# Kernel optimization log

Hardware: AMD Instinct MI355X
Metric: run time of the kernel (lower is better)

## Reference

```python
import jax, jax.numpy as jnp
import numpy as np

EMBED_DIM = 4
SEQ_LEN = 14 * 14


def setup_inputs() -> dict:
    key = jax.random.key(0)
    ks = jax.random.split(key, 7)
    B = 32768
    x = jax.random.normal(ks[0], (B, 1, 28, 28), dtype=jnp.float32)
    conv_w = jax.random.normal(ks[1], (4, 1, 2, 2), dtype=jnp.float32) * 0.5
    conv_b = jax.random.normal(ks[2], (4,), dtype=jnp.float32) * 0.1
    rotation_params = jax.random.uniform(ks[3], (16,), dtype=jnp.float32)
    entangle_params = jax.random.uniform(ks[4], (16,), dtype=jnp.float32)
    lin_w = jax.random.normal(ks[5], (10, 784), dtype=jnp.float32) * 0.05
    lin_b = jax.random.normal(ks[6], (10,), dtype=jnp.float32) * 0.05
    return {"x": x, "conv_w": conv_w, "conv_b": conv_b,
            "rotation_params": rotation_params, "entangle_params": entangle_params,
            "lin_w": lin_w, "lin_b": lin_b}


def reference(x, conv_w, conv_b, rotation_params, entangle_params, lin_w, lin_b):
    B = x.shape[0]
    # Quanvolution filter: Conv2d(1,4,k=2,s=2) -> [B,4,14,14]
    feat = jax.lax.conv_general_dilated(
        x, conv_w, window_strides=(2, 2), padding='VALID',
        dimension_numbers=('NCHW', 'OIHW', 'NCHW'))
    feat = feat + conv_b[None, :, None, None]
    # flatten (channel-major like torch .view) then reshape to [B, 196, 4]
    feat = feat.reshape(B, -1).reshape(B, SEQ_LEN, EMBED_DIM)
    # mean embedding per sample: [B, 4]
    mean_embeds = feat.mean(axis=1)
    # classical self-attention on a length-1 sequence per sample
    R = rotation_params.reshape(EMBED_DIM, EMBED_DIM)
    E = entangle_params.reshape(EMBED_DIM, EMBED_DIM)
    q = mean_embeds @ R                               # [B, 4]
    k = mean_embeds @ E                               # [B, 4]
    scores = jnp.einsum('bd,bd->b', q, k) / jnp.sqrt(jnp.float32(EMBED_DIM))
    # softmax over a single-element axis (seq_len == 1) -> all ones, kept for fidelity
    scores = jax.nn.softmax(scores[:, None], axis=-1)  # [B, 1]
    attn_weights = scores * mean_embeds                # [B, 4] (== mean_embeds)
    # broadcast-scale features and classify
    feat = (feat * attn_weights[:, None, :]).reshape(B, -1)  # [B, 784]
    logits = feat @ lin_w.T + lin_b
    return jax.nn.log_softmax(logits, axis=-1)
```

## Files before the change

### kernel.cpp

```cpp
#include <hip/hip_runtime.h>


typedef __attribute__((ext_vector_type(8))) short bf16x8;
typedef __attribute__((ext_vector_type(4))) float f32x4;
typedef __attribute__((ext_vector_type(4))) unsigned int uint4v;

union BU { uint4v u; bf16x8 b; };
union AB { unsigned int u[4]; bf16x8 b; };

__device__ __forceinline__ unsigned rne16(float f) {
  const unsigned u = __float_as_uint(f);
  return (u + 0x7FFFu + ((u >> 16) & 1u)) >> 16;
}

#define CST_F 19200
#define A_F   19240

__global__ void qsac_prep(const float* __restrict__ cw, const float* __restrict__ cb,
                          const float* __restrict__ lw, float* __restrict__ wsf) {
  unsigned short* gt = (unsigned short*)wsf;
  const int i = blockIdx.x * 256 + threadIdx.x;
  const int e = i & 7, ln = (i >> 3) & 63, c = i >> 9;
  const int t = c / 3, nt = c - t * 3;
  const int col = nt * 16 + (ln & 15);
  const int k = t * 32 + (ln >> 4) * 8 + e;
  float val = 0.f;
  if (k < 784) {
    const int r = k / 28, cc = k - r * 28;
    const int kh = r & 1, kw = cc & 1;
    const int p = (r >> 1) * 14 + (cc >> 1);
    const int dpix = (2 * ((r >> 1) & 1) + (cc >> 1)) & 3;
    const int cd = col / 12, cj = col - cd * 12;
    if (cd == dpix) {
      const float w0 = cw[(kh << 1) + kw],     w1 = cw[4 + (kh << 1) + kw],
                  w2 = cw[8 + (kh << 1) + kw], w3 = cw[12 + (kh << 1) + kw];
      if (cj < 10)
        val = w0 * lw[cj * 784 + p]       + w1 * lw[cj * 784 + 196 + p] +
              w2 * lw[cj * 784 + 392 + p] + w3 * lw[cj * 784 + 588 + p];
      else if (cj == 10)
        val = (w0 + w1 + w2 + w3) * (1.0f / 196.0f);
    }
  }
  gt[c * 512 + ln * 8 + e] = (unsigned short)rne16(val);

  if (blockIdx.x == 0) {
    const int u = threadIdx.x;
    if (u < 40) {
      const int d = u / 10, j = u - (u / 10) * 10;
      const float b0 = cb[0], b1 = cb[1], b2 = cb[2], b3 = cb[3];
      float s = 0.f;
#pragma unroll 7
      for (int q = d; q < 196; q += 4)
        s += b0 * lw[j * 784 + q]       + b1 * lw[j * 784 + 196 + q] +
             b2 * lw[j * 784 + 392 + q] + b3 * lw[j * 784 + 588 + q];
      wsf[CST_F + u] = s;
    } else if (u == 40) {
      wsf[A_F] = (cb[0] + cb[1] + cb[2] + cb[3]) * 0.25f;
    }
  }
}

__global__ __launch_bounds__(512)
__attribute__((amdgpu_waves_per_eu(4, 4))) void qsac_main(
    const float* __restrict__ x, const float* __restrict__ wsf,
    const float* __restrict__ lin_b, float* __restrict__ out) {
  __shared__ unsigned int smemu[19200];

  const int tid = threadIdx.x;
  const int lane = tid & 63;
  const int wid = __builtin_amdgcn_readfirstlane(tid >> 6);
  const int strip = wid & 3;
  const int khalf = wid >> 2;
  const int nn = lane & 15, kb = lane >> 4;
  const int sbase = blockIdx.x * 64 + strip * 16;
  const float* xrow = x + (size_t)(sbase + nn) * 784;

  {
    const char* wsb = (const char*)wsf;
#pragma unroll
    for (int i = 0; i < 10; ++i) {
      const int c = i * 8 + wid;
      if (c < 75) {
        __builtin_amdgcn_global_load_lds(
            (const __attribute__((address_space(1))) unsigned int*)
                (wsb + (size_t)(c * 64 + lane) * 16),
            (__attribute__((address_space(3))) unsigned int*)&smemu[c * 256],
            16, 0, 0);
      }
    }
  }
  __syncthreads();

  f32x4 acc[3];
#pragma unroll
  for (int nt = 0; nt < 3; ++nt) acc[nt] = (f32x4){0.f, 0.f, 0.f, 0.f};

  auto tile = [&](const float4& a, const float4& b2, int t) {
    BU bh[3];
    const unsigned int* bb = smemu + t * 768 + lane * 4;
#pragma unroll
    for (int nt = 0; nt < 3; ++nt) bh[nt].u = *(const uint4v*)(bb + nt * 256);
    AB Ah;
    Ah.u[0] = rne16(a.x)  | (rne16(a.y)  << 16);
    Ah.u[1] = rne16(a.z)  | (rne16(a.w)  << 16);
    Ah.u[2] = rne16(b2.x) | (rne16(b2.y) << 16);
    Ah.u[3] = rne16(b2.z) | (rne16(b2.w) << 16);
#pragma unroll
    for (int nt = 0; nt < 3; ++nt)
      acc[nt] = __builtin_amdgcn_mfma_f32_16x16x32_bf16(Ah.b, bh[nt].b, acc[nt], 0, 0, 0);
  };

  auto ldA = [&](int t, float4& a, float4& b2) {
    const int ka = t * 32 + kb * 8;
    const int kc = (ka < 784) ? ka : 0;
    a = *(const float4*)(xrow + kc);
    b2 = *(const float4*)(xrow + kc + 4);
  };

  const int t0 = khalf ? 12 : 0;
  const int t1 = khalf ? 25 : 12;
  float4 xa, xb, na, nb;
  ldA(t0, xa, xb);
#pragma unroll 1
  for (int t = t0; t < t1 - 1; ++t) {
    ldA(t + 1, na, nb);
    tile(xa, xb, t);
    xa = na; xb = nb;
  }
  tile(xa, xb, t1 - 1);

  __syncthreads();
  float* red = (float*)smemu;
  if (khalf == 1) {
#pragma unroll
    for (int nt = 0; nt < 3; ++nt)
#pragma unroll
      for (int rg = 0; rg < 4; ++rg)
        red[(strip * 64 + lane) * 12 + nt * 4 + rg] = acc[nt][rg];
  }
  __syncthreads();
  if (khalf == 0) {
#pragma unroll
    for (int nt = 0; nt < 3; ++nt)
#pragma unroll
      for (int rg = 0; rg < 4; ++rg)
        acc[nt][rg] += red[(strip * 64 + lane) * 12 + nt * 4 + rg];

    float* cx = (float*)smemu + 3072 + strip * (16 * 52);
#pragma unroll
    for (int nt = 0; nt < 3; ++nt)
#pragma unroll
      for (int rg = 0; rg < 4; ++rg)
        cx[(kb * 4 + rg) * 52 + nt * 16 + nn] = acc[nt][rg];
    __builtin_amdgcn_wave_barrier();

    if (lane < 16) {
      float Y[48];
#pragma unroll
      for (int q = 0; q < 12; ++q) {
        const float4 t4 = *(const float4*)&cx[lane * 52 + q * 4];
        Y[q * 4 + 0] = t4.x; Y[q * 4 + 1] = t4.y;
        Y[q * 4 + 2] = t4.z; Y[q * 4 + 3] = t4.w;
      }
      const float a = wsf[A_F];
      float M[4];
#pragma unroll
      for (int d = 0; d < 4; ++d) M[d] = a + Y[d * 12 + 10];
      float logits[10];
#pragma unroll
      for (int j = 0; j < 10; ++j) {
        float vv = lin_b[j];
#pragma unroll
        for (int d = 0; d < 4; ++d)
          vv += M[d] * (wsf[CST_F + d * 10 + j] + Y[d * 12 + j]);
        logits[j] = vv;
      }
      float mx = logits[0];
#pragma unroll
      for (int j = 1; j < 10; ++j) mx = fmaxf(mx, logits[j]);
      float se = 0.f;
#pragma unroll
      for (int j = 0; j < 10; ++j) se += __expf(logits[j] - mx);
      const float lse = mx + __logf(se);
      float* op = out + (size_t)(sbase + lane) * 10;
#pragma unroll
      for (int j = 0; j < 10; ++j) op[j] = logits[j] - lse;
    }
  }
}

extern "C" void kernel_launch(void* const* d_in, const int* in_sizes, int n_in,
                              void* d_out, int out_size, void* d_ws, size_t ws_size,
                              hipStream_t stream) {
  (void)n_in; (void)ws_size; (void)out_size;
  const float* x = (const float*)d_in[0];
  const float* conv_w = (const float*)d_in[1];
  const float* conv_b = (const float*)d_in[2];
  const float* lin_w = (const float*)d_in[5];
  const float* lin_b = (const float*)d_in[6];
  float* out = (float*)d_out;
  float* wsf = (float*)d_ws;

  hipLaunchKernelGGL(qsac_prep, dim3(150), dim3(256), 0, stream,
                     conv_w, conv_b, lin_w, wsf);

  const int B = in_sizes[0] / 784;
  const int nblk = B / 64;
  hipLaunchKernelGGL(qsac_main, dim3(nblk), dim3(512), 0, stream,
                     x, wsf, lin_b, out);
}
```

Before: 29.46 us.

## Switch to 32x32x16 MFMA with 128-sample blocks and 4-way K split

Replaces the 16x16x32 bf16 MFMA tiles with 32x32x16 MFMAs. Each block now handles 128 samples with 1024 threads: 4 strips of 32 rows and 4 K-quarters reduced through LDS. The prep kernel re-lays out the folded weight matrix into 64-column, 16-K slabs, dropping the padded-N third tile in favour of two 32-wide tiles. The aim is fewer MFMA issues and better reuse per B fragment. In exchange it adds a larger LDS footprint, a bigger cross-wave reduction with an extra barrier, and higher per-thread accumulator register pressure.

Result: slower. 32.70 us (+11.0%).

```diff
diff --git a/kernel.cpp b/kernel.cpp
--- a/kernel.cpp
+++ b/kernel.cpp
@@ -2,7 +2,7 @@
 
 
 typedef __attribute__((ext_vector_type(8))) short bf16x8;
-typedef __attribute__((ext_vector_type(4))) float f32x4;
+typedef __attribute__((ext_vector_type(16))) float f32x16;
 typedef __attribute__((ext_vector_type(4))) unsigned int uint4v;
 
 union BU { uint4v u; bf16x8 b; };
@@ -13,19 +13,19 @@
   return (u + 0x7FFFu + ((u >> 16) & 1u)) >> 16;
 }
 
-#define CST_F 19200
-#define A_F   19240
+#define CST_F 25088
+#define A_F   25128
 
 __global__ void qsac_prep(const float* __restrict__ cw, const float* __restrict__ cb,
                           const float* __restrict__ lw, float* __restrict__ wsf) {
   unsigned short* gt = (unsigned short*)wsf;
   const int i = blockIdx.x * 256 + threadIdx.x;
   const int e = i & 7, ln = (i >> 3) & 63, c = i >> 9;
-  const int t = c / 3, nt = c - t * 3;
-  const int col = nt * 16 + (ln & 15);
-  const int k = t * 32 + (ln >> 4) * 8 + e;
+  const int s = c >> 1, nt = c & 1;
+  const int col = nt * 32 + (ln & 31);
+  const int k = s * 16 + (ln >> 5) * 8 + e;
   float val = 0.f;
-  if (k < 784) {
+  if (col < 48) {
     const int r = k / 28, cc = k - r * 28;
     const int kh = r & 1, kw = cc & 1;
     const int p = (r >> 1) * 14 + (cc >> 1);
@@ -48,39 +48,40 @@
     if (u < 40) {
       const int d = u / 10, j = u - (u / 10) * 10;
       const float b0 = cb[0], b1 = cb[1], b2 = cb[2], b3 = cb[3];
-      float s = 0.f;
+      float s2 = 0.f;
 #pragma unroll 7
       for (int q = d; q < 196; q += 4)
-        s += b0 * lw[j * 784 + q]       + b1 * lw[j * 784 + 196 + q] +
-             b2 * lw[j * 784 + 392 + q] + b3 * lw[j * 784 + 588 + q];
-      wsf[CST_F + u] = s;
+        s2 += b0 * lw[j * 784 + q]       + b1 * lw[j * 784 + 196 + q] +
+              b2 * lw[j * 784 + 392 + q] + b3 * lw[j * 784 + 588 + q];
+      wsf[CST_F + u] = s2;
     } else if (u == 40) {
       wsf[A_F] = (cb[0] + cb[1] + cb[2] + cb[3]) * 0.25f;
     }
   }
 }
 
-__global__ __launch_bounds__(512)
+__global__ __launch_bounds__(1024)
 __attribute__((amdgpu_waves_per_eu(4, 4))) void qsac_main(
     const float* __restrict__ x, const float* __restrict__ wsf,
     const float* __restrict__ lin_b, float* __restrict__ out) {
-  __shared__ unsigned int smemu[19200];
+  __shared__ unsigned int smemu[25088];
 
   const int tid = threadIdx.x;
   const int lane = tid & 63;
   const int wid = __builtin_amdgcn_readfirstlane(tid >> 6);
   const int strip = wid & 3;
-  const int khalf = wid >> 2;
-  const int nn = lane & 15, kb = lane >> 4;
-  const int sbase = blockIdx.x * 64 + strip * 16;
+  const int kq = wid >> 2;
+  const int nn = lane & 31;
+  const int g = lane >> 5;
+  const int sbase = blockIdx.x * 128 + strip * 32;
   const float* xrow = x + (size_t)(sbase + nn) * 784;
 
   {
     const char* wsb = (const char*)wsf;
 #pragma unroll
-    for (int i = 0; i < 10; ++i) {
-      const int c = i * 8 + wid;
-      if (c < 75) {
+    for (int i = 0; i < 7; ++i) {
+      const int c = i * 16 + wid;
+      if (c < 98) {
         __builtin_amdgcn_global_load_lds(
             (const __attribute__((address_space(1))) unsigned int*)
                 (wsb + (size_t)(c * 64 + lane) * 16),
@@ -91,74 +92,75 @@
   }
   __syncthreads();
 
-  f32x4 acc[3];
-#pragma unroll
-  for (int nt = 0; nt < 3; ++nt) acc[nt] = (f32x4){0.f, 0.f, 0.f, 0.f};
-
-  auto tile = [&](const float4& a, const float4& b2, int t) {
-    BU bh[3];
-    const unsigned int* bb = smemu + t * 768 + lane * 4;
-#pragma unroll
-    for (int nt = 0; nt < 3; ++nt) bh[nt].u = *(const uint4v*)(bb + nt * 256);
+  f32x16 acc0, acc1;
+#pragma unroll
+  for (int r = 0; r < 16; ++r) { acc0[r] = 0.f; acc1[r] = 0.f; }
+
+  auto tile = [&](const float4& a, const float4& b2, int s) {
+    BU bh0, bh1;
+    const unsigned int* bb = smemu + s * 512 + lane * 4;
+    bh0.u = *(const uint4v*)bb;
+    bh1.u = *(const uint4v*)(bb + 256);
     AB Ah;
     Ah.u[0] = rne16(a.x)  | (rne16(a.y)  << 16);
     Ah.u[1] = rne16(a.z)  | (rne16(a.w)  << 16);
     Ah.u[2] = rne16(b2.x) | (rne16(b2.y) << 16);
     Ah.u[3] = rne16(b2.z) | (rne16(b2.w) << 16);
-#pragma unroll
-    for (int nt = 0; nt < 3; ++nt)
-      acc[nt] = __builtin_amdgcn_mfma_f32_16x16x32_bf16(Ah.b, bh[nt].b, acc[nt], 0, 0, 0);
+    acc0 = __builtin_amdgcn_mfma_f32_32x32x16_bf16(Ah.b, bh0.b, acc0, 0, 0, 0);
+    acc1 = __builtin_amdgcn_mfma_f32_32x32x16_bf16(Ah.b, bh1.b, acc1, 0, 0, 0);
   };
 
-  auto ldA = [&](int t, float4& a, float4& b2) {
-    const int ka = t * 32 + kb * 8;
-    const int kc = (ka < 784) ? ka : 0;
-    a = *(const float4*)(xrow + kc);
-    b2 = *(const float4*)(xrow + kc + 4);
+  auto ldA = [&](int s, float4& a, float4& b2) {
+    const float* p = xrow + s * 16 + g * 8;
+    a = *(const float4*)p;
+    b2 = *(const float4*)(p + 4);
   };
 
-  const int t0 = khalf ? 12 : 0;
-  const int t1 = khalf ? 25 : 12;
+  const int s0 = (kq == 0) ? 0 : 13 + (kq - 1) * 12;
+  const int s1 = s0 + ((kq == 0) ? 13 : 12);
   float4 xa, xb, na, nb;
-  ldA(t0, xa, xb);
+  ldA(s0, xa, xb);
 #pragma unroll 1
-  for (int t = t0; t < t1 - 1; ++t) {
-    ldA(t + 1, na, nb);
-    tile(xa, xb, t);
+  for (int s = s0; s < s1 - 1; ++s) {
+    ldA(s + 1, na, nb);
+    tile(xa, xb, s);
     xa = na; xb = nb;
   }
-  tile(xa, xb, t1 - 1);
+  tile(xa, xb, s1 - 1);
 
   __syncthreads();
   float* red = (float*)smemu;
-  if (khalf == 1) {
-#pragma unroll
-    for (int nt = 0; nt < 3; ++nt)
-#pragma unroll
-      for (int rg = 0; rg < 4; ++rg)
-        red[(strip * 64 + lane) * 12 + nt * 4 + rg] = acc[nt][rg];
-  }
-  __syncthreads();
-  if (khalf == 0) {
-#pragma unroll
-    for (int nt = 0; nt < 3; ++nt)
-#pragma unroll
-      for (int rg = 0; rg < 4; ++rg)
-        acc[nt][rg] += red[(strip * 64 + lane) * 12 + nt * 4 + rg];
-
-    float* cx = (float*)smemu + 3072 + strip * (16 * 52);
-#pragma unroll
-    for (int nt = 0; nt < 3; ++nt)
-#pragma unroll
-      for (int rg = 0; rg < 4; ++rg)
-        cx[(kb * 4 + rg) * 52 + nt * 16 + nn] = acc[nt][rg];
+  if (kq > 0) {
+    float* rp = red + ((strip * 3 + (kq - 1)) * 64 + lane) * 32;
+#pragma unroll
+    for (int r = 0; r < 16; ++r) { rp[r] = acc0[r]; rp[16 + r] = acc1[r]; }
+  }
+  __syncthreads();
+  if (kq == 0) {
+#pragma unroll
+    for (int q = 0; q < 3; ++q) {
+      const float* rp = red + ((strip * 3 + q) * 64 + lane) * 32;
+#pragma unroll
+      for (int r = 0; r < 16; ++r) { acc0[r] += rp[r]; acc1[r] += rp[16 + r]; }
+    }
+  }
+  __syncthreads();
+
+  if (kq == 0) {
+    float* cx = (float*)smemu + strip * (32 * 68);
+#pragma unroll
+    for (int r = 0; r < 16; ++r) {
+      const int row = (r & 3) + 8 * (r >> 2) + 4 * g;
+      cx[row * 68 + nn] = acc0[r];
+      cx[row * 68 + 32 + nn] = acc1[r];
+    }
     __builtin_amdgcn_wave_barrier();
 
-    if (lane < 16) {
+    if (lane < 32) {
       float Y[48];
 #pragma unroll
       for (int q = 0; q < 12; ++q) {
-        const float4 t4 = *(const float4*)&cx[lane * 52 + q * 4];
+        const float4 t4 = *(const float4*)&cx[lane * 68 + q * 4];
         Y[q * 4 + 0] = t4.x; Y[q * 4 + 1] = t4.y;
         Y[q * 4 + 2] = t4.z; Y[q * 4 + 3] = t4.w;
       }
@@ -201,11 +203,11 @@
   float* out = (float*)d_out;
   float* wsf = (float*)d_ws;
 
-  hipLaunchKernelGGL(qsac_prep, dim3(150), dim3(256), 0, stream,
+  hipLaunchKernelGGL(qsac_prep, dim3(196), dim3(256), 0, stream,
                      conv_w, conv_b, lin_w, wsf);
 
   const int B = in_sizes[0] / 784;
-  const int nblk = B / 64;
-  hipLaunchKernelGGL(qsac_main, dim3(nblk), dim3(512), 0, stream,
+  const int nblk = B / 128;
+  hipLaunchKernelGGL(qsac_main, dim3(nblk), dim3(1024), 0, stream,
                      x, wsf, lin_b, out);
 }
```
